# Kernel optimization log

Measured on AMD Instinct MI355X. Metric: run time of the kernel, lower is better.

Reference implementation:

```python
import jax, jax.numpy as jnp
import numpy as np

T = 16777216            # flat replay-buffer length (timesteps)
DISCOUNT = 0.99         # gamma
FINAL_REWARD = 0.0      # bootstrap value for the last timestep
TERM_PROB = 0.001       # ~1000-step episodes


def setup_inputs() -> dict:
    key = jax.random.key(0)
    k1, k2 = jax.random.split(key)
    reward = jax.random.normal(k1, (T,), dtype=jnp.float32)
    terminal = jax.random.bernoulli(k2, TERM_PROB, (T,))
    return {"terminal": terminal, "reward": reward}


def _discounted_cumret(terminal, reward):
    # Reverse-time linear recurrence (same math as tf.scan over reversed seq):
    #   c_t = r_t                      if terminal_t
    #   c_t = r_t + discount * c_{t+1} otherwise
    # i.e. c_t = a_t * c_{t+1} + b_t with a_t = discount*(1-term_t), b_t = r_t.
    # Expressed as a (log-depth) associative scan over the reversed sequence.
    a = jnp.where(terminal, jnp.zeros((), reward.dtype),
                  jnp.asarray(DISCOUNT, reward.dtype))
    a_rev = a[::-1]
    b_rev = reward[::-1]
    # fold the initializer (final_reward) into the first reversed element
    b_rev = b_rev.at[0].add(a_rev[0] * jnp.asarray(FINAL_REWARD, reward.dtype))

    def combine(e1, e2):
        # composition of affine maps x -> a*x + b (e1 applied first)
        a1, b1 = e1
        a2, b2 = e2
        return a1 * a2, a2 * b1 + b2

    _, y_rev = jax.lax.associative_scan(combine, (a_rev, b_rev))
    return y_rev[::-1]


def reference(terminal, reward):
    return _discounted_cumret(terminal, reward)
```

## Files before the change

### kernel.cpp

```cpp
#include <hip/hip_runtime.h>


constexpr int   TPB  = 256;
constexpr int   IPT  = 16;
constexpr int   TILE = TPB * IPT;
constexpr float DISC = 0.99f;

__device__ __forceinline__ void block_scan_inc(float& A, float& B,
                                               float* sA, float* sB, int t) {
    sA[t] = A; sB[t] = B;
    __syncthreads();
    #pragma unroll
    for (int off = 1; off < TPB; off <<= 1) {
        float pa = 1.f, pb = 0.f;
        if (t >= off) { pa = sA[t - off]; pb = sB[t - off]; }
        __syncthreads();
        B = A * pb + B;
        A = A * pa;
        sA[t] = A; sB[t] = B;
        __syncthreads();
    }
}

__device__ __forceinline__ void load_chunk(const int* __restrict__ term,
                                           const float* __restrict__ rew,
                                           long long base, long long T,
                                           float* r, float* a, bool fast) {
    if (fast) {
        #pragma unroll
        for (int q = 0; q < IPT / 4; ++q) {
            float4 rv = ((const float4*)(rew + base))[q];
            int4   tv = ((const int4*)(term + base))[q];
            r[4*q+0] = rv.x; r[4*q+1] = rv.y; r[4*q+2] = rv.z; r[4*q+3] = rv.w;
            a[4*q+0] = tv.x ? 0.f : DISC;
            a[4*q+1] = tv.y ? 0.f : DISC;
            a[4*q+2] = tv.z ? 0.f : DISC;
            a[4*q+3] = tv.w ? 0.f : DISC;
        }
    } else {
        #pragma unroll
        for (int k = 0; k < IPT; ++k) {
            long long i = base + k;
            if (i < T) { r[k] = rew[i]; a[k] = term[i] ? 0.f : DISC; }
            else       { r[k] = 0.f;   a[k] = 1.f; }
        }
    }
}

__global__ __launch_bounds__(TPB) void k_agg(const int* __restrict__ term,
                                             const float* __restrict__ rew,
                                             float* __restrict__ aggA,
                                             float* __restrict__ aggB,
                                             long long T) {
    __shared__ float sA[TPB], sB[TPB];
    const int t = threadIdx.x;
    const long long tileBase = (long long)blockIdx.x * TILE;
    const long long base = tileBase + (long long)(TPB - 1 - t) * IPT;

    float r[IPT], a[IPT];
    const bool fast = (base + IPT <= T);
    load_chunk(term, rew, base, T, r, a, fast);

    float A = 1.f, B = 0.f;
    #pragma unroll
    for (int k = IPT - 1; k >= 0; --k) { B = a[k] * B + r[k]; A = a[k] * A; }

    block_scan_inc(A, B, sA, sB, t);

    if (t == TPB - 1) { aggA[blockIdx.x] = A; aggB[blockIdx.x] = B; }
}

__global__ __launch_bounds__(TPB) void k_scan(const float* __restrict__ aggA,
                                              const float* __restrict__ aggB,
                                              float* __restrict__ yin,
                                              int numTiles) {
    __shared__ float sA[TPB], sB[TPB];
    const int t = threadIdx.x;
    const int cpt = (numTiles + TPB - 1) / TPB;
    const int hi = numTiles - 1 - t * cpt;

    float A = 1.f, B = 0.f;
    for (int k = 0; k < cpt; ++k) {
        int g = hi - k;
        if (g >= 0) {
            float ag = aggA[g], bg = aggB[g];
            B = ag * B + bg; A = ag * A;
        }
    }

    block_scan_inc(A, B, sA, sB, t);

    float EA = 1.f, EB = 0.f;
    if (t > 0) { EA = sA[t - 1]; EB = sB[t - 1]; }
    for (int k = 0; k < cpt; ++k) {
        int g = hi - k;
        if (g >= 0) {
            yin[g] = EB;
            float ag = aggA[g], bg = aggB[g];
            EB = ag * EB + bg; EA = ag * EA;
        }
    }
}

__global__ __launch_bounds__(TPB) void k_apply(const int* __restrict__ term,
                                               const float* __restrict__ rew,
                                               const float* __restrict__ yin,
                                               float* __restrict__ out,
                                               long long T) {
    __shared__ float sA[TPB], sB[TPB];
    const int t = threadIdx.x;
    const long long tileBase = (long long)blockIdx.x * TILE;
    const long long base = tileBase + (long long)(TPB - 1 - t) * IPT;

    float r[IPT], a[IPT];
    const bool fast = (base + IPT <= T);
    load_chunk(term, rew, base, T, r, a, fast);

    float A = 1.f, B = 0.f;
    #pragma unroll
    for (int k = IPT - 1; k >= 0; --k) { B = a[k] * B + r[k]; A = a[k] * A; }

    block_scan_inc(A, B, sA, sB, t);

    float EA = 1.f, EB = 0.f;
    if (t > 0) { EA = sA[t - 1]; EB = sB[t - 1]; }

    const float yblk = yin[blockIdx.x];
    float y = EA * yblk + EB;

    float yv[IPT];
    #pragma unroll
    for (int k = IPT - 1; k >= 0; --k) { y = a[k] * y + r[k]; yv[k] = y; }

    if (fast) {
        #pragma unroll
        for (int q = 0; q < IPT / 4; ++q) {
            ((float4*)(out + base))[q] =
                make_float4(yv[4*q+0], yv[4*q+1], yv[4*q+2], yv[4*q+3]);
        }
    } else {
        #pragma unroll
        for (int k = 0; k < IPT; ++k) {
            long long i = base + k;
            if (i < T) out[i] = yv[k];
        }
    }
}

extern "C" void kernel_launch(void* const* d_in, const int* in_sizes, int n_in,
                              void* d_out, int out_size, void* d_ws, size_t ws_size,
                              hipStream_t stream) {
    const int*   term = (const int*)d_in[0];
    const float* rew  = (const float*)d_in[1];
    float*       out  = (float*)d_out;

    const long long T = (long long)in_sizes[1];
    const int numTiles = (int)((T + TILE - 1) / TILE);

    float* aggA = (float*)d_ws;
    float* aggB = aggA + numTiles;
    float* yin  = aggB + numTiles;

    k_agg  <<<numTiles, TPB, 0, stream>>>(term, rew, aggA, aggB, T);
    k_scan <<<1,        TPB, 0, stream>>>(aggA, aggB, yin, numTiles);
    k_apply<<<numTiles, TPB, 0, stream>>>(term, rew, yin, out, T);
}
```

Measured before the change: 203.9 us.

## Replace three-kernel scan with single-pass decoupled look-back scan

Merges the aggregate, tile-scan and apply kernels into one kernel. Tiles are claimed in reverse order through an atomic counter, and each tile publishes a flagged partial aggregate and then an inclusive prefix to global memory. A 64-lane wavefront looks back over predecessor descriptors to obtain the carry-in. Inputs are now read once instead of twice, and the serial single-block scan kernel and two extra launches go away. In exchange it adds a memset, spin-waiting on cross-block flags, and a look-back latency chain.

```diff
diff --git a/kernel.cpp b/kernel.cpp
--- a/kernel.cpp
+++ b/kernel.cpp
@@ -5,6 +5,14 @@
 constexpr int   IPT  = 16;
 constexpr int   TILE = TPB * IPT;
 constexpr float DISC = 0.99f;
+
+#define FLAG_INVALID  0u
+#define FLAG_PARTIAL  1u
+#define FLAG_COMPLETE 2u
+
+__device__ __forceinline__ unsigned long long pack_desc(unsigned f, float v) {
+    return ((unsigned long long)f << 32) | (unsigned long long)__float_as_uint(v);
+}
 
 __device__ __forceinline__ void block_scan_inc(float& A, float& B,
                                                float* sA, float* sB, int t) {
@@ -22,10 +30,27 @@
     }
 }
 
-__device__ __forceinline__ void load_chunk(const int* __restrict__ term,
-                                           const float* __restrict__ rew,
-                                           long long base, long long T,
-                                           float* r, float* a, bool fast) {
+__global__ __launch_bounds__(TPB) void k_onepass(
+        const int* __restrict__ term, const float* __restrict__ rew,
+        float* __restrict__ out,
+        unsigned long long* __restrict__ w1, unsigned long long* __restrict__ w2,
+        unsigned* __restrict__ counter,
+        int numTiles, long long T) {
+    __shared__ float sA[TPB], sB[TPB];
+    __shared__ float s_Ablk, s_Bblk, s_yin;
+    __shared__ unsigned s_rank;
+
+    const int t = threadIdx.x;
+    if (t == 0) s_rank = atomicAdd(counter, 1u);
+    __syncthreads();
+    const int rank = (int)s_rank;
+    const int g = numTiles - 1 - rank;
+
+    const long long tileBase = (long long)g * TILE;
+    const long long base = tileBase + (long long)(TPB - 1 - t) * IPT;
+
+    float r[IPT], a[IPT];
+    const bool fast = (base + IPT <= T);
     if (fast) {
         #pragma unroll
         for (int q = 0; q < IPT / 4; ++q) {
@@ -45,21 +70,6 @@
             else       { r[k] = 0.f;   a[k] = 1.f; }
         }
     }
-}
-
-__global__ __launch_bounds__(TPB) void k_agg(const int* __restrict__ term,
-                                             const float* __restrict__ rew,
-                                             float* __restrict__ aggA,
-                                             float* __restrict__ aggB,
-                                             long long T) {
-    __shared__ float sA[TPB], sB[TPB];
-    const int t = threadIdx.x;
-    const long long tileBase = (long long)blockIdx.x * TILE;
-    const long long base = tileBase + (long long)(TPB - 1 - t) * IPT;
-
-    float r[IPT], a[IPT];
-    const bool fast = (base + IPT <= T);
-    load_chunk(term, rew, base, T, r, a, fast);
 
     float A = 1.f, B = 0.f;
     #pragma unroll
@@ -67,67 +77,69 @@
 
     block_scan_inc(A, B, sA, sB, t);
 
-    if (t == TPB - 1) { aggA[blockIdx.x] = A; aggB[blockIdx.x] = B; }
-}
-
-__global__ __launch_bounds__(TPB) void k_scan(const float* __restrict__ aggA,
-                                              const float* __restrict__ aggB,
-                                              float* __restrict__ yin,
-                                              int numTiles) {
-    __shared__ float sA[TPB], sB[TPB];
-    const int t = threadIdx.x;
-    const int cpt = (numTiles + TPB - 1) / TPB;
-    const int hi = numTiles - 1 - t * cpt;
-
-    float A = 1.f, B = 0.f;
-    for (int k = 0; k < cpt; ++k) {
-        int g = hi - k;
-        if (g >= 0) {
-            float ag = aggA[g], bg = aggB[g];
-            B = ag * B + bg; A = ag * A;
-        }
+    if (t == TPB - 1) {
+        s_Ablk = A; s_Bblk = B;
+        __hip_atomic_store(&w1[rank], pack_desc(FLAG_PARTIAL, A),
+                           __ATOMIC_RELAXED, __HIP_MEMORY_SCOPE_AGENT);
+        __hip_atomic_store(&w2[rank], pack_desc(FLAG_PARTIAL, B),
+                           __ATOMIC_RELEASE, __HIP_MEMORY_SCOPE_AGENT);
     }
-
-    block_scan_inc(A, B, sA, sB, t);
 
     float EA = 1.f, EB = 0.f;
     if (t > 0) { EA = sA[t - 1]; EB = sB[t - 1]; }
-    for (int k = 0; k < cpt; ++k) {
-        int g = hi - k;
-        if (g >= 0) {
-            yin[g] = EB;
-            float ag = aggA[g], bg = aggB[g];
-            EB = ag * EB + bg; EA = ag * EA;
+    __syncthreads();
+
+    if (t < 64) {
+        float accA = 1.f, accB = 0.f;
+        bool done = false;
+        float yin = 0.f;
+        for (int round = 0; !done; ++round) {
+            const int j = rank - 1 - t - round * 64;
+            float fA, fB; bool comp;
+            if (j < 0) {
+                fA = 0.f; fB = 0.f; comp = true;
+            } else {
+                unsigned long long v2 = __hip_atomic_load(
+                    &w2[j], __ATOMIC_ACQUIRE, __HIP_MEMORY_SCOPE_AGENT);
+                while ((unsigned)(v2 >> 32) == FLAG_INVALID) {
+                    __builtin_amdgcn_s_sleep(1);
+                    v2 = __hip_atomic_load(&w2[j], __ATOMIC_ACQUIRE,
+                                           __HIP_MEMORY_SCOPE_AGENT);
+                }
+                if ((unsigned)(v2 >> 32) == FLAG_COMPLETE) {
+                    comp = true; fA = 0.f; fB = __uint_as_float((unsigned)v2);
+                } else {
+                    unsigned long long v1 = __hip_atomic_load(
+                        &w1[j], __ATOMIC_RELAXED, __HIP_MEMORY_SCOPE_AGENT);
+                    comp = false;
+                    fA = __uint_as_float((unsigned)v1);
+                    fB = __uint_as_float((unsigned)v2);
+                }
+            }
+            #pragma unroll
+            for (int off = 1; off < 64; off <<= 1) {
+                float oA = __shfl_down(fA, off, 64);
+                float oB = __shfl_down(fB, off, 64);
+                if (t + off < 64) { fB = fA * oB + fB; fA = fA * oA; }
+            }
+            const bool anyComplete = (__ballot(comp) != 0ull);
+            if (t == 0) {
+                if (anyComplete) { yin = accA * fB + accB; }
+                else             { accB = accA * fB + accB; accA = accA * fA; }
+            }
+            done = anyComplete;
+        }
+        if (t == 0) {
+            s_yin = yin;
+            const float v = s_Ablk * yin + s_Bblk;
+            __hip_atomic_store(&w2[rank], pack_desc(FLAG_COMPLETE, v),
+                               __ATOMIC_RELEASE, __HIP_MEMORY_SCOPE_AGENT);
         }
     }
-}
+    __syncthreads();
+    const float yin = s_yin;
 
-__global__ __launch_bounds__(TPB) void k_apply(const int* __restrict__ term,
-                                               const float* __restrict__ rew,
-                                               const float* __restrict__ yin,
-                                               float* __restrict__ out,
-                                               long long T) {
-    __shared__ float sA[TPB], sB[TPB];
-    const int t = threadIdx.x;
-    const long long tileBase = (long long)blockIdx.x * TILE;
-    const long long base = tileBase + (long long)(TPB - 1 - t) * IPT;
-
-    float r[IPT], a[IPT];
-    const bool fast = (base + IPT <= T);
-    load_chunk(term, rew, base, T, r, a, fast);
-
-    float A = 1.f, B = 0.f;
-    #pragma unroll
-    for (int k = IPT - 1; k >= 0; --k) { B = a[k] * B + r[k]; A = a[k] * A; }
-
-    block_scan_inc(A, B, sA, sB, t);
-
-    float EA = 1.f, EB = 0.f;
-    if (t > 0) { EA = sA[t - 1]; EB = sB[t - 1]; }
-
-    const float yblk = yin[blockIdx.x];
-    float y = EA * yblk + EB;
-
+    float y = EA * yin + EB;
     float yv[IPT];
     #pragma unroll
     for (int k = IPT - 1; k >= 0; --k) { y = a[k] * y + r[k]; yv[k] = y; }
@@ -157,11 +169,13 @@
     const long long T = (long long)in_sizes[1];
     const int numTiles = (int)((T + TILE - 1) / TILE);
 
-    float* aggA = (float*)d_ws;
-    float* aggB = aggA + numTiles;
-    float* yin  = aggB + numTiles;
+    unsigned long long* w1 = (unsigned long long*)d_ws;
+    unsigned long long* w2 = w1 + numTiles;
+    unsigned* counter = (unsigned*)(w2 + numTiles);
 
-    k_agg  <<<numTiles, TPB, 0, stream>>>(term, rew, aggA, aggB, T);
-    k_scan <<<1,        TPB, 0, stream>>>(aggA, aggB, yin, numTiles);
-    k_apply<<<numTiles, TPB, 0, stream>>>(term, rew, yin, out, T);
+    const size_t ctrlBytes = (size_t)numTiles * 16 + 64;
+    hipMemsetAsync(d_ws, 0, ctrlBytes, stream);
+
+    k_onepass<<<numTiles, TPB, 0, stream>>>(term, rew, out, w1, w2, counter,
+                                            numTiles, T);
 }
```

New measurement: 761.6 us. +273.6%, slower.

## Replace LDS block scan with wave-shuffle suffix scan and shrink per-thread tiles

Applied to the files above, without the earlier changes.

Replaces the shared-memory Hillis-Steele block scan, which needs many barriers, with a 64-lane wave shuffle suffix scan plus a small cross-wave combine through LDS. Items per thread drop from 16 to 4, and threads now map to ascending addresses for better-coalesced float4 loads. Tile aggregates are packed as float2. The change trades barrier and LDS cost for four times as many tiles, so the single-block middle scan must walk a longer serial chain per thread.

```diff
diff --git a/kernel.cpp b/kernel.cpp
--- a/kernel.cpp
+++ b/kernel.cpp
@@ -2,102 +2,101 @@
 
 
 constexpr int   TPB  = 256;
-constexpr int   IPT  = 16;
+constexpr int   IPT  = 4;
 constexpr int   TILE = TPB * IPT;
 constexpr float DISC = 0.99f;
 
-__device__ __forceinline__ void block_scan_inc(float& A, float& B,
-                                               float* sA, float* sB, int t) {
-    sA[t] = A; sB[t] = B;
-    __syncthreads();
+__device__ __forceinline__ void wave_suffix_scan(float& A, float& B, int lane) {
     #pragma unroll
-    for (int off = 1; off < TPB; off <<= 1) {
-        float pa = 1.f, pb = 0.f;
-        if (t >= off) { pa = sA[t - off]; pb = sB[t - off]; }
-        __syncthreads();
-        B = A * pb + B;
-        A = A * pa;
-        sA[t] = A; sB[t] = B;
-        __syncthreads();
-    }
-}
-
-__device__ __forceinline__ void load_chunk(const int* __restrict__ term,
-                                           const float* __restrict__ rew,
-                                           long long base, long long T,
-                                           float* r, float* a, bool fast) {
-    if (fast) {
-        #pragma unroll
-        for (int q = 0; q < IPT / 4; ++q) {
-            float4 rv = ((const float4*)(rew + base))[q];
-            int4   tv = ((const int4*)(term + base))[q];
-            r[4*q+0] = rv.x; r[4*q+1] = rv.y; r[4*q+2] = rv.z; r[4*q+3] = rv.w;
-            a[4*q+0] = tv.x ? 0.f : DISC;
-            a[4*q+1] = tv.y ? 0.f : DISC;
-            a[4*q+2] = tv.z ? 0.f : DISC;
-            a[4*q+3] = tv.w ? 0.f : DISC;
-        }
-    } else {
-        #pragma unroll
-        for (int k = 0; k < IPT; ++k) {
-            long long i = base + k;
-            if (i < T) { r[k] = rew[i]; a[k] = term[i] ? 0.f : DISC; }
-            else       { r[k] = 0.f;   a[k] = 1.f; }
-        }
+    for (int off = 1; off < 64; off <<= 1) {
+        float oA = __shfl_down(A, off, 64);
+        float oB = __shfl_down(B, off, 64);
+        if (lane + off < 64) { B = A * oB + B; A = A * oA; }
     }
 }
 
 __global__ __launch_bounds__(TPB) void k_agg(const int* __restrict__ term,
                                              const float* __restrict__ rew,
-                                             float* __restrict__ aggA,
-                                             float* __restrict__ aggB,
+                                             float2* __restrict__ agg,
                                              long long T) {
-    __shared__ float sA[TPB], sB[TPB];
+    __shared__ float2 sW[TPB / 64];
     const int t = threadIdx.x;
-    const long long tileBase = (long long)blockIdx.x * TILE;
-    const long long base = tileBase + (long long)(TPB - 1 - t) * IPT;
+    const int lane = t & 63, wav = t >> 6;
+    const long long base = (long long)blockIdx.x * TILE + (long long)t * IPT;
 
     float r[IPT], a[IPT];
-    const bool fast = (base + IPT <= T);
-    load_chunk(term, rew, base, T, r, a, fast);
+    if (base + IPT <= T) {
+        float4 rv = *(const float4*)(rew + base);
+        int4   tv = *(const int4*)(term + base);
+        r[0]=rv.x; r[1]=rv.y; r[2]=rv.z; r[3]=rv.w;
+        a[0]=tv.x?0.f:DISC; a[1]=tv.y?0.f:DISC; a[2]=tv.z?0.f:DISC; a[3]=tv.w?0.f:DISC;
+    } else {
+        #pragma unroll
+        for (int k = 0; k < IPT; ++k) {
+            long long i = base + k;
+            if (i < T) { r[k]=rew[i]; a[k]=term[i]?0.f:DISC; }
+            else       { r[k]=0.f;   a[k]=1.f; }
+        }
+    }
 
     float A = 1.f, B = 0.f;
     #pragma unroll
-    for (int k = IPT - 1; k >= 0; --k) { B = a[k] * B + r[k]; A = a[k] * A; }
+    for (int k = IPT - 1; k >= 0; --k) { B = a[k]*B + r[k]; A = a[k]*A; }
 
-    block_scan_inc(A, B, sA, sB, t);
-
-    if (t == TPB - 1) { aggA[blockIdx.x] = A; aggB[blockIdx.x] = B; }
+    wave_suffix_scan(A, B, lane);
+    if (lane == 0) sW[wav] = make_float2(A, B);
+    __syncthreads();
+    if (t == 0) {
+        float2 g = sW[0];
+        #pragma unroll
+        for (int w = 1; w < TPB / 64; ++w) {
+            float2 h = sW[w];
+            g.y = g.x * h.y + g.y; g.x = g.x * h.x;
+        }
+        agg[blockIdx.x] = g;
+    }
 }
 
-__global__ __launch_bounds__(TPB) void k_scan(const float* __restrict__ aggA,
-                                              const float* __restrict__ aggB,
-                                              float* __restrict__ yin,
-                                              int numTiles) {
-    __shared__ float sA[TPB], sB[TPB];
+__global__ __launch_bounds__(TPB) void k_mid(const float2* __restrict__ agg,
+                                             float* __restrict__ yin,
+                                             int numTiles) {
+    __shared__ float2 sW[TPB / 64];
     const int t = threadIdx.x;
+    const int lane = t & 63, wav = t >> 6;
     const int cpt = (numTiles + TPB - 1) / TPB;
-    const int hi = numTiles - 1 - t * cpt;
+    const int lo = t * cpt;
 
     float A = 1.f, B = 0.f;
-    for (int k = 0; k < cpt; ++k) {
-        int g = hi - k;
-        if (g >= 0) {
-            float ag = aggA[g], bg = aggB[g];
-            B = ag * B + bg; A = ag * A;
+    for (int k = cpt - 1; k >= 0; --k) {
+        int g = lo + k;
+        if (g < numTiles) {
+            float2 v = agg[g];
+            B = v.x * B + v.y; A = v.x * A;
         }
     }
 
-    block_scan_inc(A, B, sA, sB, t);
+    float IA = A, IB = B;
+    wave_suffix_scan(IA, IB, lane);
+    if (lane == 0) sW[wav] = make_float2(IA, IB);
+    __syncthreads();
 
-    float EA = 1.f, EB = 0.f;
-    if (t > 0) { EA = sA[t - 1]; EB = sB[t - 1]; }
-    for (int k = 0; k < cpt; ++k) {
-        int g = hi - k;
-        if (g >= 0) {
-            yin[g] = EB;
-            float ag = aggA[g], bg = aggB[g];
-            EB = ag * EB + bg; EA = ag * EA;
+    float EWA = 1.f, EWB = 0.f;
+    #pragma unroll
+    for (int w = 0; w < TPB / 64; ++w)
+        if (w > wav) { float2 h = sW[w]; EWB = EWA*h.y + EWB; EWA = EWA*h.x; }
+
+    float EA = __shfl_down(IA, 1, 64);
+    float EB = __shfl_down(IB, 1, 64);
+    if (lane == 63) { EA = 1.f; EB = 0.f; }
+
+    float x1 = EWB;
+    float v  = EA * x1 + EB;
+    for (int k = cpt - 1; k >= 0; --k) {
+        int g = lo + k;
+        if (g < numTiles) {
+            yin[g] = v;
+            float2 q = agg[g];
+            v = q.x * v + q.y;
         }
     }
 }
@@ -107,37 +106,55 @@
                                                const float* __restrict__ yin,
                                                float* __restrict__ out,
                                                long long T) {
-    __shared__ float sA[TPB], sB[TPB];
+    __shared__ float2 sW[TPB / 64];
     const int t = threadIdx.x;
-    const long long tileBase = (long long)blockIdx.x * TILE;
-    const long long base = tileBase + (long long)(TPB - 1 - t) * IPT;
+    const int lane = t & 63, wav = t >> 6;
+    const long long base = (long long)blockIdx.x * TILE + (long long)t * IPT;
 
     float r[IPT], a[IPT];
     const bool fast = (base + IPT <= T);
-    load_chunk(term, rew, base, T, r, a, fast);
+    if (fast) {
+        float4 rv = *(const float4*)(rew + base);
+        int4   tv = *(const int4*)(term + base);
+        r[0]=rv.x; r[1]=rv.y; r[2]=rv.z; r[3]=rv.w;
+        a[0]=tv.x?0.f:DISC; a[1]=tv.y?0.f:DISC; a[2]=tv.z?0.f:DISC; a[3]=tv.w?0.f:DISC;
+    } else {
+        #pragma unroll
+        for (int k = 0; k < IPT; ++k) {
+            long long i = base + k;
+            if (i < T) { r[k]=rew[i]; a[k]=term[i]?0.f:DISC; }
+            else       { r[k]=0.f;   a[k]=1.f; }
+        }
+    }
 
     float A = 1.f, B = 0.f;
     #pragma unroll
-    for (int k = IPT - 1; k >= 0; --k) { B = a[k] * B + r[k]; A = a[k] * A; }
+    for (int k = IPT - 1; k >= 0; --k) { B = a[k]*B + r[k]; A = a[k]*A; }
 
-    block_scan_inc(A, B, sA, sB, t);
+    float IA = A, IB = B;
+    wave_suffix_scan(IA, IB, lane);
+    if (lane == 0) sW[wav] = make_float2(IA, IB);
+    __syncthreads();
 
-    float EA = 1.f, EB = 0.f;
-    if (t > 0) { EA = sA[t - 1]; EB = sB[t - 1]; }
+    float EWA = 1.f, EWB = 0.f;
+    #pragma unroll
+    for (int w = 0; w < TPB / 64; ++w)
+        if (w > wav) { float2 h = sW[w]; EWB = EWA*h.y + EWB; EWA = EWA*h.x; }
 
-    const float yblk = yin[blockIdx.x];
-    float y = EA * yblk + EB;
+    float EA = __shfl_down(IA, 1, 64);
+    float EB = __shfl_down(IB, 1, 64);
+    if (lane == 63) { EA = 1.f; EB = 0.f; }
+
+    const float yt = yin[blockIdx.x];
+    float x1 = EWA * yt + EWB;
+    float y  = EA * x1 + EB;
 
     float yv[IPT];
     #pragma unroll
-    for (int k = IPT - 1; k >= 0; --k) { y = a[k] * y + r[k]; yv[k] = y; }
+    for (int k = IPT - 1; k >= 0; --k) { y = a[k]*y + r[k]; yv[k] = y; }
 
     if (fast) {
-        #pragma unroll
-        for (int q = 0; q < IPT / 4; ++q) {
-            ((float4*)(out + base))[q] =
-                make_float4(yv[4*q+0], yv[4*q+1], yv[4*q+2], yv[4*q+3]);
-        }
+        *(float4*)(out + base) = make_float4(yv[0], yv[1], yv[2], yv[3]);
     } else {
         #pragma unroll
         for (int k = 0; k < IPT; ++k) {
@@ -157,11 +174,10 @@
     const long long T = (long long)in_sizes[1];
     const int numTiles = (int)((T + TILE - 1) / TILE);
 
-    float* aggA = (float*)d_ws;
-    float* aggB = aggA + numTiles;
-    float* yin  = aggB + numTiles;
+    float2* agg = (float2*)d_ws;
+    float*  yin = (float*)(agg + numTiles);
 
-    k_agg  <<<numTiles, TPB, 0, stream>>>(term, rew, aggA, aggB, T);
-    k_scan <<<1,        TPB, 0, stream>>>(aggA, aggB, yin, numTiles);
+    k_agg  <<<numTiles, TPB, 0, stream>>>(term, rew, agg, T);
+    k_mid  <<<1,        TPB, 0, stream>>>(agg, yin, numTiles);
     k_apply<<<numTiles, TPB, 0, stream>>>(term, rew, yin, out, T);
 }
```

Result: slower. 215.5 us (+5.7%).
